# Kernel optimization log

Hardware: AMD Instinct MI355X
Metric: run time of the kernel (lower is better)

## Reference

```python
import jax, jax.numpy as jnp
import numpy as np

DIM = 64     # qudit dimension (size of M)
WIRES = 3    # total qudits; full Hilbert dim D = DIM**WIRES = 262144
INDEX = 1    # wire the custom gate acts on
BATCH = 128  # number of state columns


def setup_inputs() -> dict:
    key = jax.random.key(0)
    k1, k2, k3, k4 = jax.random.split(key, 4)
    D = DIM ** WIRES
    return {
        "M_real": jax.random.normal(k1, (DIM, DIM), dtype=jnp.float32),
        "M_imag": jax.random.normal(k2, (DIM, DIM), dtype=jnp.float32),
        "x_real": jax.random.normal(k3, (D, BATCH), dtype=jnp.float32),
        "x_imag": jax.random.normal(k4, (D, BATCH), dtype=jnp.float32),
    }


def reference(M_real, M_imag, x_real, x_imag):
    # Original torch code builds U = I_{dim^index} (x) M (x) I_{dim^(wires-index-1)}
    # via iterative kron, then computes U @ x. Mathematically identical and
    # exponentially cheaper: reshape x to expose the target qudit axis and
    # contract M only along that axis (tensor-network style).
    M = jax.lax.complex(M_real, M_imag)          # (dim, dim) complex64
    x = jax.lax.complex(x_real, x_imag)          # (D, B) complex64
    B = x.shape[1]
    left = DIM ** INDEX                          # dims before target wire
    right = DIM ** (WIRES - INDEX - 1)           # dims after target wire
    xr = x.reshape(left, DIM, right, B)          # (a, j, r, b)
    y = jnp.einsum('ij,ajrb->airb', M, xr)       # apply M on the target axis
    return y.reshape(DIM ** WIRES, B)            # same as (kron U) @ x
```

## Files before the change

### kernel.cpp

```cpp
#include <hip/hip_runtime.h>

#define DIMQ   64
#define NCOLS  8192
#define SLAB   (DIMQ * NCOLS)
#define NA     64
#define DB     (NA * SLAB)

typedef __attribute__((ext_vector_type(8))) __bf16 bf16x8;
typedef __attribute__((ext_vector_type(8))) unsigned short us8;
typedef __attribute__((ext_vector_type(4))) float f32x4;

__device__ __forceinline__ unsigned short f2bf(float f) {
    unsigned u = __builtin_bit_cast(unsigned, f);
    unsigned r = u + 0x7fffu + ((u >> 16) & 1u);
    return (unsigned short)(r >> 16);
}

__device__ __forceinline__ void load_M_frags(
    const float* __restrict__ Mr, const float* __restrict__ Mi,
    int l15, int q, bf16x8 fMr[4][2], bf16x8 fMi[4][2])
{
#pragma unroll
    for (int it = 0; it < 4; ++it) {
#pragma unroll
        for (int kb = 0; kb < 2; ++kb) {
            const int row = it * 16 + l15;
            const int col = kb * 32 + q * 8;
            const float* pr = Mr + row * DIMQ + col;
            const float* pi = Mi + row * DIMQ + col;
            us8 hr, hi;
#pragma unroll
            for (int j = 0; j < 8; ++j) {
                hr[j] = f2bf(pr[j]);
                hi[j] = f2bf(pi[j]);
            }
            fMr[it][kb] = __builtin_bit_cast(bf16x8, hr);
            fMi[it][kb] = __builtin_bit_cast(bf16x8, hi);
        }
    }
}

__global__ __launch_bounds__(64, 2) void gate_real_kernel(
    const float* __restrict__ Mr, const float* __restrict__ Mi,
    const float* __restrict__ Xr, const float* __restrict__ Xi,
    float* __restrict__ Out)
{
    const int lane = threadIdx.x;
    const int l15  = lane & 15;
    const int q    = lane >> 4;

    bf16x8 fMr[4][2], fMi[4][2];
    load_M_frags(Mr, Mi, l15, q, fMr, fMi);

    const int bid = blockIdx.x;
    const int a   = bid >> 6;
    const int nch = bid & 63;
    const size_t baseA = (size_t)a * SLAB;

    for (int tt = 0; tt < 8; ++tt) {
        const int n0 = nch * 128 + tt * 16;
        f32x4 accR[4] = {f32x4{0,0,0,0}, f32x4{0,0,0,0}, f32x4{0,0,0,0}, f32x4{0,0,0,0}};

#pragma unroll
        for (int kb = 0; kb < 2; ++kb) {
            const int krow = kb * 32 + q * 8;
            const float* pr = Xr + baseA + (size_t)krow * NCOLS + n0 + l15;
            const float* pi = Xi + baseA + (size_t)krow * NCOLS + n0 + l15;
            float fr[8], fi[8];
#pragma unroll
            for (int j = 0; j < 8; ++j) {
                fr[j] = pr[(size_t)j * NCOLS];
                fi[j] = pi[(size_t)j * NCOLS];
            }
            us8 hr, hni;
#pragma unroll
            for (int j = 0; j < 8; ++j) {
                hr[j]  = f2bf(fr[j]);
                hni[j] = (unsigned short)(f2bf(fi[j]) ^ 0x8000u);
            }
            const bf16x8 bXr  = __builtin_bit_cast(bf16x8, hr);
            const bf16x8 bXni = __builtin_bit_cast(bf16x8, hni);

#pragma unroll
            for (int it = 0; it < 4; ++it) {
                accR[it] = __builtin_amdgcn_mfma_f32_16x16x32_bf16(fMr[it][kb], bXr,  accR[it], 0, 0, 0);
                accR[it] = __builtin_amdgcn_mfma_f32_16x16x32_bf16(fMi[it][kb], bXni, accR[it], 0, 0, 0);
            }
        }

#pragma unroll
        for (int it = 0; it < 4; ++it) {
#pragma unroll
            for (int r = 0; r < 4; ++r) {
                const int i = it * 16 + q * 4 + r;
                Out[baseA + (size_t)i * NCOLS + n0 + l15] = accR[it][r];
            }
        }
    }
}

__global__ __launch_bounds__(64, 2) void gate_cplx_kernel(
    const float* __restrict__ Mr, const float* __restrict__ Mi,
    const float* __restrict__ Xr, const float* __restrict__ Xi,
    float* __restrict__ Out)
{
    const int lane = threadIdx.x;
    const int l15  = lane & 15;
    const int q    = lane >> 4;

    bf16x8 fMr[4][2], fMi[4][2];
    load_M_frags(Mr, Mi, l15, q, fMr, fMi);

    const int bid = blockIdx.x;
    const int a   = bid >> 6;
    const int nch = bid & 63;
    const size_t baseA = (size_t)a * SLAB;

    for (int tt = 0; tt < 8; ++tt) {
        const int n0 = nch * 128 + tt * 16;
        f32x4 accR[4] = {f32x4{0,0,0,0}, f32x4{0,0,0,0}, f32x4{0,0,0,0}, f32x4{0,0,0,0}};
        f32x4 accI[4] = {f32x4{0,0,0,0}, f32x4{0,0,0,0}, f32x4{0,0,0,0}, f32x4{0,0,0,0}};

#pragma unroll
        for (int kb = 0; kb < 2; ++kb) {
            const int krow = kb * 32 + q * 8;
            const float* pr = Xr + baseA + (size_t)krow * NCOLS + n0 + l15;
            const float* pi = Xi + baseA + (size_t)krow * NCOLS + n0 + l15;
            float fr[8], fi[8];
#pragma unroll
            for (int j = 0; j < 8; ++j) {
                fr[j] = pr[(size_t)j * NCOLS];
                fi[j] = pi[(size_t)j * NCOLS];
            }
            us8 hr, hi, hni;
#pragma unroll
            for (int j = 0; j < 8; ++j) {
                hr[j] = f2bf(fr[j]);
                const unsigned short t = f2bf(fi[j]);
                hi[j]  = t;
                hni[j] = (unsigned short)(t ^ 0x8000u);
            }
            const bf16x8 bXr  = __builtin_bit_cast(bf16x8, hr);
            const bf16x8 bXi  = __builtin_bit_cast(bf16x8, hi);
            const bf16x8 bXni = __builtin_bit_cast(bf16x8, hni);

#pragma unroll
            for (int it = 0; it < 4; ++it) {
                accR[it] = __builtin_amdgcn_mfma_f32_16x16x32_bf16(fMr[it][kb], bXr,  accR[it], 0, 0, 0);
                accR[it] = __builtin_amdgcn_mfma_f32_16x16x32_bf16(fMi[it][kb], bXni, accR[it], 0, 0, 0);
                accI[it] = __builtin_amdgcn_mfma_f32_16x16x32_bf16(fMr[it][kb], bXi,  accI[it], 0, 0, 0);
                accI[it] = __builtin_amdgcn_mfma_f32_16x16x32_bf16(fMi[it][kb], bXr,  accI[it], 0, 0, 0);
            }
        }

#pragma unroll
        for (int it = 0; it < 4; ++it) {
#pragma unroll
            for (int r = 0; r < 4; ++r) {
                const int i = it * 16 + q * 4 + r;
                const size_t cidx = baseA + (size_t)i * NCOLS + n0 + l15;
                float2 v;
                v.x = accR[it][r];
                v.y = accI[it][r];
                reinterpret_cast<float2*>(Out)[cidx] = v;
            }
        }
    }
}

extern "C" void kernel_launch(void* const* d_in, const int* in_sizes, int n_in,
                              void* d_out, int out_size, void* d_ws, size_t ws_size,
                              hipStream_t stream) {
    const float* Mr = (const float*)d_in[0];
    const float* Mi = (const float*)d_in[1];
    const float* Xr = (const float*)d_in[2];
    const float* Xi = (const float*)d_in[3];
    float* Out = (float*)d_out;

    dim3 grid(NA * 64);
    dim3 block(64);
    if (out_size >= 2 * DB) {
        gate_cplx_kernel<<<grid, block, 0, stream>>>(Mr, Mi, Xr, Xi, Out);
    } else {
        gate_real_kernel<<<grid, block, 0, stream>>>(Mr, Mi, Xr, Xi, Out);
    }
}
```

Measured before the change: 366.3 us.

## Stage X tiles into LDS via direct global-to-LDS loads in 4-wave blocks

The real-output kernel now runs 256-thread blocks, each handling a 64-column chunk of one slab. It stages the full 64x64 tile of X real and imaginary into padded LDS with global_load_lds 16-byte loads, then each wave reads its K fragments from LDS instead of issuing strided scalar global loads. This targets the uncoalesced 4-byte column-strided global reads of the old kernel and its low occupancy from 64-thread blocks. In exchange it adds about 33KB of LDS per block and a block barrier, and drops the per-block loop over column tiles.

```diff
diff --git a/kernel.cpp b/kernel.cpp
--- a/kernel.cpp
+++ b/kernel.cpp
@@ -5,6 +5,10 @@
 #define SLAB   (DIMQ * NCOLS)
 #define NA     64
 #define DB     (NA * SLAB)
+
+#define CHUNKB 1040
+#define NCHUNK 16
+#define ARRB   (NCHUNK * CHUNKB)
 
 typedef __attribute__((ext_vector_type(8))) __bf16 bf16x8;
 typedef __attribute__((ext_vector_type(8))) unsigned short us8;
@@ -40,61 +44,87 @@
     }
 }
 
-__global__ __launch_bounds__(64, 2) void gate_real_kernel(
+__global__ __launch_bounds__(256, 4) void gate_real_v2(
     const float* __restrict__ Mr, const float* __restrict__ Mi,
     const float* __restrict__ Xr, const float* __restrict__ Xi,
     float* __restrict__ Out)
 {
-    const int lane = threadIdx.x;
+    __shared__ __align__(16) char lds[2 * ARRB];
+
+    const int tid  = threadIdx.x;
+    const int lane = tid & 63;
+    const int w    = tid >> 6;
     const int l15  = lane & 15;
     const int q    = lane >> 4;
 
+    const int bid   = blockIdx.x;
+    const int a     = bid >> 7;
+    const int chunk = bid & 127;
+    const int n0blk = chunk * 64;
+    const size_t baseA = (size_t)a * SLAB;
+
+    {
+        const float* gR = Xr + baseA + n0blk;
+        const float* gI = Xi + baseA + n0blk;
+        char* ldsR = lds;
+        char* ldsI = lds + ARRB;
+#pragma unroll
+        for (int pl = 0; pl < 4; ++pl) {
+            const int p   = w * 4 + pl;
+            const int row = p * 4 + (lane >> 4);
+            const size_t goff = (size_t)row * NCOLS + (size_t)(lane & 15) * 4;
+            __builtin_amdgcn_global_load_lds(
+                (const __attribute__((address_space(1))) void*)(gR + goff),
+                (__attribute__((address_space(3))) void*)(ldsR + p * CHUNKB),
+                16, 0, 0);
+            __builtin_amdgcn_global_load_lds(
+                (const __attribute__((address_space(1))) void*)(gI + goff),
+                (__attribute__((address_space(3))) void*)(ldsI + p * CHUNKB),
+                16, 0, 0);
+        }
+    }
+
     bf16x8 fMr[4][2], fMi[4][2];
     load_M_frags(Mr, Mi, l15, q, fMr, fMi);
 
-    const int bid = blockIdx.x;
-    const int a   = bid >> 6;
-    const int nch = bid & 63;
-    const size_t baseA = (size_t)a * SLAB;
-
-    for (int tt = 0; tt < 8; ++tt) {
-        const int n0 = nch * 128 + tt * 16;
-        f32x4 accR[4] = {f32x4{0,0,0,0}, f32x4{0,0,0,0}, f32x4{0,0,0,0}, f32x4{0,0,0,0}};
-
-#pragma unroll
-        for (int kb = 0; kb < 2; ++kb) {
-            const int krow = kb * 32 + q * 8;
-            const float* pr = Xr + baseA + (size_t)krow * NCOLS + n0 + l15;
-            const float* pi = Xi + baseA + (size_t)krow * NCOLS + n0 + l15;
-            float fr[8], fi[8];
-#pragma unroll
-            for (int j = 0; j < 8; ++j) {
-                fr[j] = pr[(size_t)j * NCOLS];
-                fi[j] = pi[(size_t)j * NCOLS];
-            }
-            us8 hr, hni;
-#pragma unroll
-            for (int j = 0; j < 8; ++j) {
-                hr[j]  = f2bf(fr[j]);
-                hni[j] = (unsigned short)(f2bf(fi[j]) ^ 0x8000u);
-            }
-            const bf16x8 bXr  = __builtin_bit_cast(bf16x8, hr);
-            const bf16x8 bXni = __builtin_bit_cast(bf16x8, hni);
-
-#pragma unroll
-            for (int it = 0; it < 4; ++it) {
-                accR[it] = __builtin_amdgcn_mfma_f32_16x16x32_bf16(fMr[it][kb], bXr,  accR[it], 0, 0, 0);
-                accR[it] = __builtin_amdgcn_mfma_f32_16x16x32_bf16(fMi[it][kb], bXni, accR[it], 0, 0, 0);
-            }
-        }
+    __syncthreads();
+
+    const int c = w * 16 + l15;
+    f32x4 acc[4] = {f32x4{0,0,0,0}, f32x4{0,0,0,0}, f32x4{0,0,0,0}, f32x4{0,0,0,0}};
+
+#pragma unroll
+    for (int kb = 0; kb < 2; ++kb) {
+        const int k0 = kb * 32 + q * 8;
+        float fr[8], fi[8];
+#pragma unroll
+        for (int j = 0; j < 8; ++j) {
+            const int k   = k0 + j;
+            const int off = (k >> 2) * CHUNKB + (k & 3) * 256 + c * 4;
+            fr[j] = *(const float*)(lds + off);
+            fi[j] = *(const float*)(lds + ARRB + off);
+        }
+        us8 hr, hni;
+#pragma unroll
+        for (int j = 0; j < 8; ++j) {
+            hr[j]  = f2bf(fr[j]);
+            hni[j] = (unsigned short)(f2bf(fi[j]) ^ 0x8000u);
+        }
+        const bf16x8 bXr  = __builtin_bit_cast(bf16x8, hr);
+        const bf16x8 bXni = __builtin_bit_cast(bf16x8, hni);
 
 #pragma unroll
         for (int it = 0; it < 4; ++it) {
-#pragma unroll
-            for (int r = 0; r < 4; ++r) {
-                const int i = it * 16 + q * 4 + r;
-                Out[baseA + (size_t)i * NCOLS + n0 + l15] = accR[it][r];
-            }
+            acc[it] = __builtin_amdgcn_mfma_f32_16x16x32_bf16(fMr[it][kb], bXr,  acc[it], 0, 0, 0);
+            acc[it] = __builtin_amdgcn_mfma_f32_16x16x32_bf16(fMi[it][kb], bXni, acc[it], 0, 0, 0);
+        }
+    }
+
+#pragma unroll
+    for (int it = 0; it < 4; ++it) {
+#pragma unroll
+        for (int r = 0; r < 4; ++r) {
+            const int i = it * 16 + q * 4 + r;
+            Out[baseA + (size_t)i * NCOLS + n0blk + c] = acc[it][r];
         }
     }
 }
@@ -177,11 +207,13 @@
     const float* Xi = (const float*)d_in[3];
     float* Out = (float*)d_out;
 
-    dim3 grid(NA * 64);
-    dim3 block(64);
     if (out_size >= 2 * DB) {
+        dim3 grid(NA * 64);
+        dim3 block(64);
         gate_cplx_kernel<<<grid, block, 0, stream>>>(Mr, Mi, Xr, Xi, Out);
     } else {
-        gate_real_kernel<<<grid, block, 0, stream>>>(Mr, Mi, Xr, Xi, Out);
-    }
-}
+        dim3 grid(NA * 128);
+        dim3 block(256);
+        gate_real_v2<<<grid, block, 0, stream>>>(Mr, Mi, Xr, Xi, Out);
+    }
+}
```

New measurement: 461.2 us. 25.9% more time.
